# Performance work log

Hardware: AMD Instinct MI355X
Metric: run time of the kernel (lower is better)

## Reference

```python
import jax, jax.numpy as jnp
import numpy as np

# Config (scaled-down DeepSeek-style MoE)
B, S, H = 4, 1024, 1024       # batch, seq, hidden_size
I = 512                        # intermediate_size per expert
E = 64                         # num_routed_experts
K = 8                          # top-k
C = 1024
NS = 1                         # num_shared_experts


def setup_inputs() -> dict:
    key = jax.random.key(0)
    ks = jax.random.split(key, 8)
    def w(k, shape, fan_in):
        return jax.random.normal(k, shape, jnp.float32) / np.float32(np.sqrt(fan_in))
    return {
        "hidden_states": jax.random.normal(ks[0], (B, S, H), jnp.float32),
        "gate_w":    w(ks[1], (E, H), H),            # nn.Linear(H, E).weight
        "shared_wg": w(ks[2], (I * NS, H), H),       # shared SwiGLU gate_proj
        "shared_wu": w(ks[3], (I * NS, H), H),       # shared SwiGLU up_proj
        "shared_wd": w(ks[4], (H, I * NS), I * NS),  # shared SwiGLU down_proj
        "expert_wg": w(ks[5], (E, I, H), H),         # routed gate_proj, stacked
        "expert_wu": w(ks[6], (E, I, H), H),         # routed up_proj, stacked
        "expert_wd": w(ks[7], (E, H, I), I),         # routed down_proj, stacked
    }


def reference(hidden_states, gate_w, shared_wg, shared_wu, shared_wd,
              expert_wg, expert_wu, expert_wd):
    b, s, h = hidden_states.shape
    x = hidden_states.reshape(-1, h)                     # [T, H]
    T = x.shape[0]

    # ---- shared expert (SwiGLU) ----
    shared = (jax.nn.silu(x @ shared_wg.T) * (x @ shared_wu.T)) @ shared_wd.T

    # ---- gating: sigmoid scores, top-k, normalize by sum ----
    scores = jax.nn.sigmoid(x @ gate_w.T)                # [T, E]
    topw, topi = jax.lax.top_k(scores, K)                # [T, K]
    topw = topw / topw.sum(-1, keepdims=True)

    # ---- dispatch: position of each (token, slot) within its expert ----
    e_flat = topi.reshape(-1)                            # [N] expert id per routed row
    N = e_flat.shape[0]
    order = jnp.argsort(e_flat)                          # rows sorted by expert id
    sorted_e = e_flat[order]
    seg_start = jnp.searchsorted(sorted_e, jnp.arange(E))
    pos_sorted = (jnp.arange(N) - seg_start[sorted_e]).astype(jnp.int32)
    pos = jnp.zeros(N, jnp.int32).at[order].set(pos_sorted)  # slot within expert buffer

    tok = jnp.repeat(jnp.arange(T), K)                   # token id per routed row
    xin = x[tok]                                         # [N, H]

    # scatter tokens into per-expert buffers [E, C, H]
    buf = jnp.zeros((E, C, h), x.dtype).at[e_flat, pos].set(xin, mode='drop')

    # per-expert SwiGLU via batched GEMMs (grouped-GEMM equivalent)
    g = jax.nn.silu(jnp.einsum('ech,eih->eci', buf, expert_wg))
    u = jnp.einsum('ech,eih->eci', buf, expert_wu)
    out_buf = jnp.einsum('eci,ehi->ech', g * u, expert_wd)  # [E, C, H]

    # gather back and combine with normalized top-k weights
    rows = out_buf[e_flat, pos]                          # [N, H]
    routed = (rows.reshape(T, K, h) * topw[..., None]).sum(1)

    return (shared + routed).reshape(b, s, h)
```

## Files before the change

### kernel.cpp

```cpp
#include <hip/hip_runtime.h>
#include <hip/hip_bf16.h>

#define TOK 4096
#define HD 1024
#define ID 512
#define NE 64
#define TK 8
#define CAP 1024
#define NROUTE 32768
#define NCHUNK 128

typedef __attribute__((ext_vector_type(4))) float f32x4;
typedef __attribute__((ext_vector_type(8))) short s16x8;
typedef __attribute__((ext_vector_type(2))) __bf16 bf16x2;

__device__ __forceinline__ ushort f2bf(float f){
  uint u = __builtin_bit_cast(uint, f);
  u += 0x7fffu + ((u >> 16) & 1u);
  return (ushort)(u >> 16);
}
__device__ __forceinline__ float bf2f(ushort b){
  uint u = ((uint)b) << 16;
  return __builtin_bit_cast(float, u);
}
__device__ __forceinline__ uint2 f4_to_bf4(float4 v){
  bf16x2 p0; p0[0] = (__bf16)v.x; p0[1] = (__bf16)v.y;
  bf16x2 p1; p1[0] = (__bf16)v.z; p1[1] = (__bf16)v.w;
  uint2 r; r.x = __builtin_bit_cast(uint, p0); r.y = __builtin_bit_cast(uint, p1);
  return r;
}
__device__ __forceinline__ short bfs(float f){
  __bf16 h = (__bf16)f;
  return __builtin_bit_cast(short, h);
}
__device__ __forceinline__ s16x8 pack8(f32x4 a, f32x4 b){
  s16x8 r;
  r[0]=bfs(a[0]); r[1]=bfs(a[1]); r[2]=bfs(a[2]); r[3]=bfs(a[3]);
  r[4]=bfs(b[0]); r[5]=bfs(b[1]); r[6]=bfs(b[2]); r[7]=bfs(b[3]);
  return r;
}
__device__ __forceinline__ void gld16(void* lds, const void* g){
  __builtin_amdgcn_global_load_lds((const __attribute__((address_space(1))) unsigned int*)g,
                                   (__attribute__((address_space(3))) unsigned int*)lds, 16, 0, 0);
}

__global__ __launch_bounds__(256)
void gating_kernel(const float* __restrict__ X, const float* __restrict__ GW,
                   ushort* __restrict__ Xbf,
                   int* __restrict__ topi, float* __restrict__ topw)
{
  __shared__ float xt[16][68];
  __shared__ float gt[64][68];
  __shared__ double ds[16][72];
  const int tid = threadIdx.x;
  const int tbase = blockIdx.x * 16;
  const int t = tid & 15, e0 = (tid >> 4) * 4;
  double acc[4] = {0.0, 0.0, 0.0, 0.0};
  for (int hc=0; hc<HD; hc+=64){
    { int r = tid >> 4, c4 = (tid & 15) * 4;
      float4 v = *(const float4*)(X + (size_t)(tbase+r)*HD + hc + c4);
      *(float4*)&xt[r][c4] = v;
      *(uint2*)(Xbf + (size_t)(tbase+r)*HD + hc + c4) = f4_to_bf4(v);
    }
    #pragma unroll
    for (int it=0; it<4; ++it){
      int idx = it*256 + tid;
      int r = idx >> 4, c4 = (idx & 15) * 4;
      *(float4*)&gt[r][c4] = *(const float4*)(GW + (size_t)r*HD + hc + c4);
    }
    __syncthreads();
    #pragma unroll
    for (int k4=0; k4<16; ++k4){
      float4 xv = *(const float4*)&xt[t][k4*4];
      #pragma unroll
      for (int j=0;j<4;++j){
        float4 gv = *(const float4*)&gt[e0+j][k4*4];
        acc[j] += (double)xv.x*(double)gv.x + (double)xv.y*(double)gv.y
                + (double)xv.z*(double)gv.z + (double)xv.w*(double)gv.w;
      }
    }
    __syncthreads();
  }
  #pragma unroll
  for (int j=0;j<4;++j) ds[t][e0+j] = acc[j];
  __syncthreads();
  if (tid < 16){
    int tt = tid;
    int idxs[8]; double vals[8]; double sum = 0.0;
    #pragma unroll
    for (int k=0;k<8;++k){
      double best = -1e300; int bi = 0;
      for (int e=0;e<NE;++e){ double v = ds[tt][e]; if (v > best){ best = v; bi = e; } }
      ds[tt][bi] = -1e300;
      double w = 1.0 / (1.0 + exp(-best));
      idxs[k] = bi; vals[k] = w; sum += w;
    }
    double inv = 1.0 / sum;
    #pragma unroll
    for (int k=0;k<8;++k){
      topi[(size_t)(tbase+tt)*TK + k] = idxs[k];
      topw[(size_t)(tbase+tt)*TK + k] = (float)(vals[k]*inv);
    }
  }
}

__global__ __launch_bounds__(256)
void hist_kernel(const int* __restrict__ topi, int* __restrict__ ccnt){
  __shared__ int h[NE];
  const int tid = threadIdx.x;
  if (tid < NE) h[tid] = 0;
  __syncthreads();
  atomicAdd(&h[topi[blockIdx.x*256 + tid]], 1);
  __syncthreads();
  if (tid < NE) ccnt[blockIdx.x*NE + tid] = h[tid];
}

__global__ __launch_bounds__(64)
void scan_kernel(const int* __restrict__ ccnt, int* __restrict__ cbase,
                 int* __restrict__ cntC, int* __restrict__ ebase){
  const int e = threadIdx.x;
  int run = 0;
  for (int c=0;c<NCHUNK;++c){ cbase[c*NE+e] = run; run += ccnt[c*NE+e]; }
  cntC[e] = run < CAP ? run : CAP;
  __syncthreads();
  if (e == 0){
    int s = 0;
    for (int i=0;i<NE;++i){ ebase[i] = s; s += cntC[i]; }
    ebase[NE] = s;
  }
}

__global__ __launch_bounds__(64)
void assign_kernel(const int* __restrict__ topi, const int* __restrict__ cbase,
                   int* __restrict__ pos, int* __restrict__ rowlist){
  __shared__ int es[256];
  const int tid = threadIdx.x;
  const int c = blockIdx.x;
  for (int i=tid;i<256;i+=64) es[i] = topi[c*256+i];
  __syncthreads();
  const int e = tid;
  int cntr = cbase[c*NE+e];
  for (int j=0;j<256;++j){
    if (es[j] == e){
      int n = c*256+j;
      pos[n] = cntr;
      if (cntr < CAP) rowlist[e*CAP + cntr] = n;
      ++cntr;
    }
  }
}

__global__ __launch_bounds__(256,2)
void gateup_kernel(const ushort* __restrict__ Xbf,
                   const float* __restrict__ WG, const float* __restrict__ WU,
                   const float* __restrict__ SWG, const float* __restrict__ SWU,
                   const int* __restrict__ rowlist, const int* __restrict__ cntC,
                   const int* __restrict__ ebase,
                   ushort* __restrict__ interm_r, ushort* __restrict__ interm_s)
{
  int nt, mt, cnt, outbase;
  const float *wg, *wu;
  ushort* interm;
  const bool shared_p = (blockIdx.x >= 4096u);
  const int e_rl = shared_p ? 0 : ((((blockIdx.x >> 3) >> 6) << 3) | (blockIdx.x & 7));
  if (shared_p){
    int b = blockIdx.x - 4096;
    nt = b & 7; mt = b >> 3; cnt = TOK; outbase = mt*128;
    wg = SWG + (size_t)nt*64*HD; wu = SWU + (size_t)nt*64*HD;
    interm = interm_s;
  } else {
    int rem = blockIdx.x >> 3;
    nt = rem & 7; mt = (rem >> 3) & 7;
    cnt = cntC[e_rl];
    if (mt*128 >= cnt) return;
    outbase = ebase[e_rl] + mt*128;
    const size_t wof = (size_t)e_rl*ID*HD;
    wg = WG + wof + (size_t)nt*64*HD; wu = WU + wof + (size_t)nt*64*HD;
    interm = interm_r;
  }

  __shared__ ushort aL[64*128];
  __shared__ float  bF[128*64];
  __shared__ int tokb[128];

  const int tid = threadIdx.x;
  if (tid < 128){
    int tokv;
    if (shared_p) tokv = mt*128 + tid;
    else tokv = (mt*128 + tid < cnt) ? (rowlist[e_rl*CAP + mt*128 + tid] >> 3) : 0;
    tokb[tid] = tokv;
  }
  __syncthreads();

  const int w = tid >> 6, l = tid & 63;
  const int wm = w >> 1, wn = w & 1;
  const int fr = l & 15, fko = (l >> 4) * 8;

  const ushort* aSrc[4];
  #pragma unroll
  for (int j=0;j<4;++j){
    int f = j*256 + tid;
    int L = f >> 4, s = f & 15;
    int g = s ^ (L & 15);
    int row = 2*L + (g >> 3);
    aSrc[j] = Xbf + (size_t)tokb[row]*HD + (g & 7)*8;
  }
  const float* bSrc[8];
  #pragma unroll
  for (int j=0;j<8;++j){
    int f = j*256 + tid;
    int R = f >> 4, s = f & 15;
    int g = s ^ (R & 15);
    const float* base = (j < 4) ? wg : wu;
    int r2 = (j < 4) ? R : (R - 64);
    bSrc[j] = base + (size_t)r2*HD + g*4;
  }

  f32x4 accg[4][2], accu[4][2];
  #pragma unroll
  for (int i=0;i<4;++i)
    #pragma unroll
    for (int j=0;j<2;++j){ accg[i][j] = (f32x4)0.0f; accu[i][j] = (f32x4)0.0f; }

  auto stage = [&](int kc){
    #pragma unroll
    for (int j=0;j<4;++j) gld16(aL + (size_t)(j*256 + w*64)*8, aSrc[j] + kc);
    #pragma unroll
    for (int j=0;j<8;++j) gld16(bF + (size_t)(j*256 + w*64)*4, bSrc[j] + kc);
  };

  stage(0);
  for (int kc=0; kc<HD; kc+=64){
    __syncthreads();
    #pragma unroll
    for (int ks=0; ks<2; ++ks){
      s16x8 a[4];
      #pragma unroll
      for (int mb=0; mb<4; ++mb){
        int r = wm*64 + mb*16 + fr;
        int agl = ks*4 + (fko >> 3);
        int g = ((r & 1) << 3) | agl;
        int L = r >> 1;
        int gs = g ^ (L & 15);
        a[mb] = *(const s16x8*)&aL[L*128 + gs*8];
      }
      #pragma unroll
      for (int cg=0; cg<2; ++cg){
        int Rg = wn*32 + cg*16 + fr;
        int gl0 = ks*8 + (fko >> 2);
        int x0 = Rg*64 + ((gl0 ^ (Rg & 15)) * 4);
        int x1 = Rg*64 + (((gl0+1) ^ (Rg & 15)) * 4);
        s16x8 bg = pack8(*(const f32x4*)&bF[x0], *(const f32x4*)&bF[x1]);
        int Ru = 64 + wn*32 + cg*16 + fr;
        int y0 = Ru*64 + ((gl0 ^ (Ru & 15)) * 4);
        int y1 = Ru*64 + (((gl0+1) ^ (Ru & 15)) * 4);
        s16x8 bu = pack8(*(const f32x4*)&bF[y0], *(const f32x4*)&bF[y1]);
        #pragma unroll
        for (int mb=0; mb<4; ++mb){
          accg[mb][cg] = __builtin_amdgcn_mfma_f32_16x16x32_bf16(a[mb], bg, accg[mb][cg], 0, 0, 0);
          accu[mb][cg] = __builtin_amdgcn_mfma_f32_16x16x32_bf16(a[mb], bu, accu[mb][cg], 0, 0, 0);
        }
      }
    }
    __syncthreads();
    if (kc + 64 < HD) stage(kc + 64);
  }

  const int rq = (l >> 4) * 4;
  #pragma unroll
  for (int mb=0; mb<4; ++mb){
    #pragma unroll
    for (int q=0; q<4; ++q){
      int rloc = wm*64 + mb*16 + rq + q;
      if (mt*128 + rloc >= cnt) continue;
      size_t orow = (size_t)(outbase + rloc);
      #pragma unroll
      for (int cg=0; cg<2; ++cg){
        float g = accg[mb][cg][q], u = accu[mb][cg][q];
        float sv = g / (1.0f + __expf(-g)) * u;
        interm[orow*ID + (size_t)(nt*64 + wn*32 + cg*16 + fr)] = f2bf(sv);
      }
    }
  }
}

__global__ __launch_bounds__(256,2)
void down_kernel(const ushort* __restrict__ interm_r, const ushort* __restrict__ interm_s,
                 const float* __restrict__ WD, const float* __restrict__ SWD,
                 const int* __restrict__ cntC, const int* __restrict__ ebase,
                 ushort* __restrict__ out_rows, float* __restrict__ outf)
{
  int nt, mt, cnt, abase;
  const ushort* A;
  const float* wd;
  const bool shared_p = (blockIdx.x >= 4096u);
  if (shared_p){
    int b = blockIdx.x - 4096;
    nt = b & 7; mt = b >> 3; cnt = TOK; abase = mt*128;
    A = interm_s + (size_t)abase*ID;
    wd = SWD + (size_t)nt*128*ID;
  } else {
    int x = blockIdx.x & 7; int rem = blockIdx.x >> 3;
    nt = rem & 7; mt = (rem >> 3) & 7; int e = ((rem >> 6) << 3) | x;
    cnt = cntC[e];
    if (mt*128 >= cnt) return;
    abase = ebase[e] + mt*128;
    A = interm_r + (size_t)abase*ID;
    wd = WD + (size_t)e*HD*ID + (size_t)nt*128*ID;
  }

  __shared__ ushort aL[64*128];
  __shared__ float  bF[128*64];

  const int tid = threadIdx.x;
  const int w = tid >> 6, l = tid & 63;
  const int wm = w >> 1, wn = w & 1;
  const int fr = l & 15, fko = (l >> 4) * 8;

  const ushort* aSrc[4];
  #pragma unroll
  for (int j=0;j<4;++j){
    int f = j*256 + tid;
    int L = f >> 4, s = f & 15;
    int g = s ^ (L & 15);
    int row = 2*L + (g >> 3);
    aSrc[j] = A + (size_t)row*ID + (g & 7)*8;
  }
  const float* bSrc[8];
  #pragma unroll
  for (int j=0;j<8;++j){
    int f = j*256 + tid;
    int R = f >> 4, s = f & 15;
    int g = s ^ (R & 15);
    bSrc[j] = wd + (size_t)R*ID + g*4;
  }

  f32x4 acc[4][4];
  #pragma unroll
  for (int i=0;i<4;++i)
    #pragma unroll
    for (int j=0;j<4;++j) acc[i][j] = (f32x4)0.0f;

  auto stage = [&](int kc){
    #pragma unroll
    for (int j=0;j<4;++j) gld16(aL + (size_t)(j*256 + w*64)*8, aSrc[j] + kc);
    #pragma unroll
    for (int j=0;j<8;++j) gld16(bF + (size_t)(j*256 + w*64)*4, bSrc[j] + kc);
  };

  stage(0);
  for (int kc=0; kc<ID; kc+=64){
    __syncthreads();
    #pragma unroll
    for (int ks=0; ks<2; ++ks){
      s16x8 a[4];
      #pragma unroll
      for (int mb=0; mb<4; ++mb){
        int r = wm*64 + mb*16 + fr;
        int agl = ks*4 + (fko >> 3);
        int g = ((r & 1) << 3) | agl;
        int L = r >> 1;
        int gs = g ^ (L & 15);
        a[mb] = *(const s16x8*)&aL[L*128 + gs*8];
      }
      #pragma unroll
      for (int cg=0; cg<4; ++cg){
        int R = wn*64 + cg*16 + fr;
        int gl0 = ks*8 + (fko >> 2);
        int x0 = R*64 + ((gl0 ^ (R & 15)) * 4);
        int x1 = R*64 + (((gl0+1) ^ (R & 15)) * 4);
        s16x8 bd = pack8(*(const f32x4*)&bF[x0], *(const f32x4*)&bF[x1]);
        #pragma unroll
        for (int mb=0; mb<4; ++mb){
          acc[mb][cg] = __builtin_amdgcn_mfma_f32_16x16x32_bf16(a[mb], bd, acc[mb][cg], 0, 0, 0);
        }
      }
    }
    __syncthreads();
    if (kc + 64 < ID) stage(kc + 64);
  }

  const int rq = (l >> 4) * 4;
  #pragma unroll
  for (int mb=0; mb<4; ++mb){
    #pragma unroll
    for (int q=0; q<4; ++q){
      int rloc = wm*64 + mb*16 + rq + q;
      if (mt*128 + rloc >= cnt) continue;
      #pragma unroll
      for (int cg=0; cg<4; ++cg){
        float v = acc[mb][cg][q];
        int colg = nt*128 + wn*64 + cg*16 + fr;
        if (shared_p) outf[(size_t)(mt*128 + rloc)*HD + colg] = v;
        else          out_rows[(size_t)(abase + rloc)*HD + colg] = f2bf(v);
      }
    }
  }
}

__global__ __launch_bounds__(256)
void combine_kernel(const int* __restrict__ topi, const float* __restrict__ topw,
                    const int* __restrict__ pos, const int* __restrict__ ebase,
                    const ushort* __restrict__ out_rows, float* __restrict__ out)
{
  const int t = blockIdx.x;
  const int tid = threadIdx.x;
  __shared__ int rws[TK];
  __shared__ float wts[TK];
  if (tid < TK){
    int e = topi[(size_t)t*TK + tid];
    int p = pos[(size_t)t*TK + tid];
    rws[tid] = (p < CAP) ? (ebase[e] + p) : -1;
    wts[tid] = topw[(size_t)t*TK + tid];
  }
  __syncthreads();
  const int h0 = tid * 4;
  float4 acc = *(float4*)(out + (size_t)t*HD + h0);
  #pragma unroll
  for (int k=0;k<TK;++k){
    int r = rws[k];
    if (r < 0) continue;
    ushort4 v = *(const ushort4*)(out_rows + (size_t)r*HD + h0);
    float wk = wts[k];
    acc.x += wk*bf2f(v.x); acc.y += wk*bf2f(v.y);
    acc.z += wk*bf2f(v.z); acc.w += wk*bf2f(v.w);
  }
  *(float4*)(out + (size_t)t*HD + h0) = acc;
}

extern "C" void kernel_launch(void* const* d_in, const int* in_sizes, int n_in,
                              void* d_out, int out_size, void* d_ws, size_t ws_size,
                              hipStream_t stream)
{
  (void)in_sizes; (void)n_in; (void)out_size; (void)ws_size;
  const float* X   = (const float*)d_in[0];
  const float* GW  = (const float*)d_in[1];
  const float* SWG = (const float*)d_in[2];
  const float* SWU = (const float*)d_in[3];
  const float* SWD = (const float*)d_in[4];
  const float* EWG = (const float*)d_in[5];
  const float* EWU = (const float*)d_in[6];
  const float* EWD = (const float*)d_in[7];
  float* OUT = (float*)d_out;

  char* p = (char*)d_ws;
  int*    topi    = (int*)p;      p += (size_t)NROUTE*4;
  float*  topw    = (float*)p;    p += (size_t)NROUTE*4;
  int*    pos     = (int*)p;      p += (size_t)NROUTE*4;
  int*    ccnt    = (int*)p;      p += (size_t)NCHUNK*NE*4;
  int*    cbase   = (int*)p;      p += (size_t)NCHUNK*NE*4;
  int*    cntC    = (int*)p;      p += 256;
  int*    ebase   = (int*)p;      p += 512;
  int*    rowlist = (int*)p;      p += (size_t)NE*CAP*4;
  ushort* Xbf     = (ushort*)p;   p += (size_t)TOK*HD*2;
  ushort* interm_r= (ushort*)p;   p += (size_t)(NROUTE+128)*ID*2;
  ushort* interm_s= (ushort*)p;   p += (size_t)TOK*ID*2;
  ushort* out_rows= (ushort*)p;   p += (size_t)NROUTE*HD*2;

  gating_kernel<<<256, 256, 0, stream>>>(X, GW, Xbf, topi, topw);
  hist_kernel<<<NCHUNK, 256, 0, stream>>>(topi, ccnt);
  scan_kernel<<<1, 64, 0, stream>>>(ccnt, cbase, cntC, ebase);
  assign_kernel<<<NCHUNK, 64, 0, stream>>>(topi, cbase, pos, rowlist);

  gateup_kernel<<<4352, 256, 0, stream>>>(Xbf, EWG, EWU, SWG, SWU,
                                          rowlist, cntC, ebase, interm_r, interm_s);
  down_kernel<<<4352, 256, 0, stream>>>(interm_r, interm_s, EWD, SWD,
                                        cntC, ebase, out_rows, OUT);

  combine_kernel<<<TOK, 256, 0, stream>>>(topi, topw, pos, ebase, out_rows, OUT);
}
```

Measured before the change: 361.5 us.

## Fuse top-k combine into down-projection epilogue via atomic adds

The down-projection kernel now scales each output row by its routing weight and atomically adds it into the final fp32 output at the owning token's row. This removes the bf16 out_rows intermediate buffer and the separate combine kernel, along with their global write and read traffic. The output is zeroed with a memset first, since the shared-expert blocks also accumulate atomically. In exchange, every output element gets up to nine fp32 atomic adds, and the summation order becomes nondeterministic.

Result: slower. 404.3 us (+11.8%).

```diff
diff --git a/kernel.cpp b/kernel.cpp
--- a/kernel.cpp
+++ b/kernel.cpp
@@ -288,9 +288,10 @@
 void down_kernel(const ushort* __restrict__ interm_r, const ushort* __restrict__ interm_s,
                  const float* __restrict__ WD, const float* __restrict__ SWD,
                  const int* __restrict__ cntC, const int* __restrict__ ebase,
-                 ushort* __restrict__ out_rows, float* __restrict__ outf)
+                 const int* __restrict__ rowlist, const float* __restrict__ topw,
+                 float* __restrict__ outf)
 {
-  int nt, mt, cnt, abase;
+  int nt, mt, cnt, abase, e_rl = 0;
   const ushort* A;
   const float* wd;
   const bool shared_p = (blockIdx.x >= 4096u);
@@ -301,18 +302,30 @@
     wd = SWD + (size_t)nt*128*ID;
   } else {
     int x = blockIdx.x & 7; int rem = blockIdx.x >> 3;
-    nt = rem & 7; mt = (rem >> 3) & 7; int e = ((rem >> 6) << 3) | x;
-    cnt = cntC[e];
+    nt = rem & 7; mt = (rem >> 3) & 7; e_rl = ((rem >> 6) << 3) | x;
+    cnt = cntC[e_rl];
     if (mt*128 >= cnt) return;
-    abase = ebase[e] + mt*128;
+    abase = ebase[e_rl] + mt*128;
     A = interm_r + (size_t)abase*ID;
-    wd = WD + (size_t)e*HD*ID + (size_t)nt*128*ID;
+    wd = WD + (size_t)e_rl*HD*ID + (size_t)nt*128*ID;
   }
 
   __shared__ ushort aL[64*128];
   __shared__ float  bF[128*64];
+  __shared__ int   tokb[128];
+  __shared__ float wrow[128];
 
   const int tid = threadIdx.x;
+  if (tid < 128){
+    if (shared_p){
+      tokb[tid] = mt*128 + tid; wrow[tid] = 1.0f;
+    } else if (mt*128 + tid < cnt){
+      int n = rowlist[e_rl*CAP + mt*128 + tid];
+      tokb[tid] = n >> 3; wrow[tid] = topw[n];
+    } else { tokb[tid] = 0; wrow[tid] = 0.0f; }
+  }
+  __syncthreads();
+
   const int w = tid >> 6, l = tid & 63;
   const int wm = w >> 1, wn = w & 1;
   const int fr = l & 15, fko = (l >> 4) * 8;
@@ -387,45 +400,16 @@
     for (int q=0; q<4; ++q){
       int rloc = wm*64 + mb*16 + rq + q;
       if (mt*128 + rloc >= cnt) continue;
+      int tok = tokb[rloc];
+      float wv = wrow[rloc];
       #pragma unroll
       for (int cg=0; cg<4; ++cg){
-        float v = acc[mb][cg][q];
+        float v = acc[mb][cg][q] * wv;
         int colg = nt*128 + wn*64 + cg*16 + fr;
-        if (shared_p) outf[(size_t)(mt*128 + rloc)*HD + colg] = v;
-        else          out_rows[(size_t)(abase + rloc)*HD + colg] = f2bf(v);
-      }
-    }
-  }
-}
-
-__global__ __launch_bounds__(256)
-void combine_kernel(const int* __restrict__ topi, const float* __restrict__ topw,
-                    const int* __restrict__ pos, const int* __restrict__ ebase,
-                    const ushort* __restrict__ out_rows, float* __restrict__ out)
-{
-  const int t = blockIdx.x;
-  const int tid = threadIdx.x;
-  __shared__ int rws[TK];
-  __shared__ float wts[TK];
-  if (tid < TK){
-    int e = topi[(size_t)t*TK + tid];
-    int p = pos[(size_t)t*TK + tid];
-    rws[tid] = (p < CAP) ? (ebase[e] + p) : -1;
-    wts[tid] = topw[(size_t)t*TK + tid];
-  }
-  __syncthreads();
-  const int h0 = tid * 4;
-  float4 acc = *(float4*)(out + (size_t)t*HD + h0);
-  #pragma unroll
-  for (int k=0;k<TK;++k){
-    int r = rws[k];
-    if (r < 0) continue;
-    ushort4 v = *(const ushort4*)(out_rows + (size_t)r*HD + h0);
-    float wk = wts[k];
-    acc.x += wk*bf2f(v.x); acc.y += wk*bf2f(v.y);
-    acc.z += wk*bf2f(v.z); acc.w += wk*bf2f(v.w);
-  }
-  *(float4*)(out + (size_t)t*HD + h0) = acc;
+        atomicAdd(&outf[(size_t)tok*HD + colg], v);
+      }
+    }
+  }
 }
 
 extern "C" void kernel_launch(void* const* d_in, const int* in_sizes, int n_in,
@@ -455,8 +439,8 @@
   ushort* Xbf     = (ushort*)p;   p += (size_t)TOK*HD*2;
   ushort* interm_r= (ushort*)p;   p += (size_t)(NROUTE+128)*ID*2;
   ushort* interm_s= (ushort*)p;   p += (size_t)TOK*ID*2;
-  ushort* out_rows= (ushort*)p;   p += (size_t)NROUTE*HD*2;
-
+
+  hipMemsetAsync(OUT, 0, (size_t)TOK*HD*4, stream);
   gating_kernel<<<256, 256, 0, stream>>>(X, GW, Xbf, topi, topw);
   hist_kernel<<<NCHUNK, 256, 0, stream>>>(topi, ccnt);
   scan_kernel<<<1, 64, 0, stream>>>(ccnt, cbase, cntC, ebase);
@@ -465,7 +449,5 @@
   gateup_kernel<<<4352, 256, 0, stream>>>(Xbf, EWG, EWU, SWG, SWU,
                                           rowlist, cntC, ebase, interm_r, interm_s);
   down_kernel<<<4352, 256, 0, stream>>>(interm_r, interm_s, EWD, SWD,
-                                        cntC, ebase, out_rows, OUT);
-
-  combine_kernel<<<TOK, 256, 0, stream>>>(topi, topw, pos, ebase, out_rows, OUT);
-}
+                                        cntC, ebase, rowlist, topw, OUT);
+}
```
